# Performance work log

Hardware: AMD Instinct MI355X
Metric: run time of the kernel (lower is better)

Reference implementation:

```python
import jax, jax.numpy as jnp
import numpy as np

NUM_HEADS = 16
EMBED_DIM = 1024
HEAD_DIM = EMBED_DIM // NUM_HEADS


def setup_inputs() -> dict:
    key = jax.random.key(0)
    kq, kk, kv, kw, kb = jax.random.split(key, 5)
    B, S, D = 2, 2048, EMBED_DIM
    bound = 1.0 / np.sqrt(D)
    return {
        "query": jax.random.normal(kq, (B, S, D), dtype=jnp.float32),
        "key": jax.random.normal(kk, (B, S, D), dtype=jnp.float32),
        "value": jax.random.normal(kv, (B, S, D), dtype=jnp.float32),
        "W_out": jax.random.uniform(kw, (D, D), minval=-bound, maxval=bound, dtype=jnp.float32),
        "b_out": jax.random.uniform(kb, (D,), minval=-bound, maxval=bound, dtype=jnp.float32),
        "prelu_a": jnp.array(0.25, dtype=jnp.float32),
    }


def reference(query, key, value, W_out, b_out, prelu_a):
    B, S, D = query.shape
    # Note: the original forward never applies q/k/v linear layers, only reshape.
    q = query.reshape(B, S, NUM_HEADS, HEAD_DIM)  # b s h d
    k = key.reshape(B, S, NUM_HEADS, HEAD_DIM)
    v = value.reshape(B, S, NUM_HEADS, HEAD_DIM)
    scale = 1.0 / np.sqrt(HEAD_DIM).astype(np.float32)
    scores = jnp.einsum("bqhd,bkhd->bhqk", q, k) * scale  # [B,H,S,S]
    attn = jax.nn.softmax(scores, axis=-1)
    out = jnp.einsum("bhqk,bkhd->bqhd", attn, v).reshape(B, S, D)
    out = out @ W_out.T + b_out  # torch Linear: x @ W.T + b
    # dropout is identity in eval mode; PReLU with single scalar param
    out = jnp.where(out >= 0, out, prelu_a * out)
    return out
```

## Files before the change

### kernel.cpp

```cpp
#include <hip/hip_runtime.h>
#include <hip/hip_bf16.h>

typedef __attribute__((ext_vector_type(8))) short bf16x8;
typedef __attribute__((ext_vector_type(4))) float f32x4;

#define S_LEN 2048
#define EMB   1024
#define NH    16
#define HD    64

__device__ inline int swz(int row, int chunk) {
  return row * 64 + ((chunk ^ (row & 7)) << 3);
}

__device__ inline int swz128(int row, int chunk) {
  return row * 128 + ((chunk ^ (row & 15)) << 3);
}

__device__ inline int kperm(int s) {
  return (s & 0x23) | ((s & 0x04) << 2) | ((s & 0x18) >> 1);
}

__device__ inline uint4 cvt8(const float* __restrict__ src, float scale) {
  float4 f0 = ((const float4*)src)[0];
  float4 f1 = ((const float4*)src)[1];
  __hip_bfloat16 t[8];
  t[0] = __float2bfloat16(f0.x * scale);
  t[1] = __float2bfloat16(f0.y * scale);
  t[2] = __float2bfloat16(f0.z * scale);
  t[3] = __float2bfloat16(f0.w * scale);
  t[4] = __float2bfloat16(f1.x * scale);
  t[5] = __float2bfloat16(f1.y * scale);
  t[6] = __float2bfloat16(f1.z * scale);
  t[7] = __float2bfloat16(f1.w * scale);
  return *(uint4*)t;
}

__device__ inline uint4 cvt8r(float4 f0, float4 f1) {
  __hip_bfloat16 t[8];
  t[0] = __float2bfloat16(f0.x);
  t[1] = __float2bfloat16(f0.y);
  t[2] = __float2bfloat16(f0.z);
  t[3] = __float2bfloat16(f0.w);
  t[4] = __float2bfloat16(f1.x);
  t[5] = __float2bfloat16(f1.y);
  t[6] = __float2bfloat16(f1.z);
  t[7] = __float2bfloat16(f1.w);
  return *(uint4*)t;
}

__device__ inline void ld8f(const float* __restrict__ p, float4& a, float4& b) {
  a = ((const float4*)p)[0];
  b = ((const float4*)p)[1];
}

__global__ __launch_bounds__(256)
void prep(const float* __restrict__ V, __hip_bfloat16* __restrict__ Vt) {
  __shared__ float vt[64 * 65];
  const int tid = threadIdx.x;
  const int st = blockIdx.x, h = blockIdx.y, b = blockIdx.z;
  const size_t srcbase = ((size_t)(b * S_LEN + st * 64)) * EMB + h * HD;
  const size_t vtb = ((size_t)(b * NH + h) * HD) * S_LEN + st * 64;

  for (int c = tid; c < 512; c += 256) {
    const int r = c >> 3, c8 = (c & 7) * 8;
    const float* vsrc = V + srcbase + (size_t)r * EMB + c8;
    float4 a = ((const float4*)vsrc)[0];
    float4 d4 = ((const float4*)vsrc)[1];
    float tv[8] = {a.x, a.y, a.z, a.w, d4.x, d4.y, d4.z, d4.w};
    #pragma unroll
    for (int j = 0; j < 8; ++j) vt[r * 65 + c8 + j] = tv[j];
  }
  __syncthreads();
  for (int c = tid; c < 512; c += 256) {
    const int d = c >> 3, s8 = (c & 7) * 8;
    __hip_bfloat16 t[8];
    #pragma unroll
    for (int j = 0; j < 8; ++j)
      t[j] = __float2bfloat16(vt[(s8 + j) * 65 + d]);
    *(uint4*)(Vt + vtb + (size_t)d * S_LEN + s8) = *(uint4*)t;
  }
}

__global__ __launch_bounds__(512, 4)
void attn_fwd(const float* __restrict__ Q,
              const float* __restrict__ K,
              const __hip_bfloat16* __restrict__ Vt,
              __hip_bfloat16* __restrict__ O)
{
  __shared__ __align__(16) __hip_bfloat16 qs[128 * 64];
  __shared__ __align__(16) __hip_bfloat16 ks[2][128 * 64];
  __shared__ __align__(16) __hip_bfloat16 vs[2][64 * 128];

  const int qt   = blockIdx.x;
  const int h    = blockIdx.y;
  const int b    = blockIdx.z;
  const int tid  = threadIdx.x;
  const int wave = tid >> 6;
  const int lane = tid & 63;
  const int ln   = lane & 15;
  const int qd   = lane >> 4;

  const size_t baseQ = ((size_t)(b * S_LEN + qt * 128)) * EMB + h * HD;
  const size_t baseK = ((size_t)(b * S_LEN)) * EMB + h * HD;
  const size_t vtb   = ((size_t)(b * NH + h) * HD) * S_LEN;

  const int r0 = tid >> 3, cc = tid & 7;
  const int kpos0 = swz(kperm(r0), cc);
  const int kpos1 = kpos0 + 64 * 64;
  const int vr0 = tid >> 4, vch = tid & 15;
  const int vpos0 = swz128(vr0, vch);
  const int vpos1 = vpos0 + 32 * 128;

  float4 ka0, kb0, ka1, kb1;
  ld8f(K + baseK + (size_t)(r0)      * EMB + cc * 8, ka0, kb0);
  ld8f(K + baseK + (size_t)(64 + r0) * EMB + cc * 8, ka1, kb1);
  uint4 vreg0 = *(const uint4*)(Vt + vtb + (size_t)vr0        * S_LEN + vch * 8);
  uint4 vreg1 = *(const uint4*)(Vt + vtb + (size_t)(vr0 + 32) * S_LEN + vch * 8);

  const float qscale = 0.125f * 1.44269504088896f;
  #pragma unroll
  for (int i = 0; i < 2; ++i) {
    const int c = tid + 512 * i, row = c >> 3, ch = c & 7;
    *(uint4*)&qs[swz(row, ch)] = cvt8(Q + baseQ + (size_t)row * EMB + ch * 8, qscale);
  }
  *(uint4*)&ks[0][kpos0] = cvt8r(ka0, kb0);
  *(uint4*)&ks[0][kpos1] = cvt8r(ka1, kb1);
  *(uint4*)&vs[0][vpos0] = vreg0;
  *(uint4*)&vs[0][vpos1] = vreg1;
  ld8f(K + baseK + (size_t)(128 + r0) * EMB + cc * 8, ka0, kb0);
  ld8f(K + baseK + (size_t)(192 + r0) * EMB + cc * 8, ka1, kb1);
  vreg0 = *(const uint4*)(Vt + vtb + (size_t)vr0        * S_LEN + 128 + vch * 8);
  vreg1 = *(const uint4*)(Vt + vtb + (size_t)(vr0 + 32) * S_LEN + 128 + vch * 8);
  __syncthreads();

  bf16x8 aq[2];
  #pragma unroll
  for (int kh = 0; kh < 2; ++kh)
    aq[kh] = *(const bf16x8*)&qs[swz(wave * 16 + ln, kh * 4 + qd)];

  bf16x8 ones;
  #pragma unroll
  for (int j = 0; j < 8; ++j) ones[j] = (short)0x3F80;

  f32x4 oacc[4] = {};
  f32x4 lacc = {};

  for (int kt = 0; kt < S_LEN / 128; ++kt) {
    const int cur = kt & 1;
    if (kt + 1 < S_LEN / 128) {
      *(uint4*)&ks[1 - cur][kpos0] = cvt8r(ka0, kb0);
      *(uint4*)&ks[1 - cur][kpos1] = cvt8r(ka1, kb1);
      *(uint4*)&vs[1 - cur][vpos0] = vreg0;
      *(uint4*)&vs[1 - cur][vpos1] = vreg1;
      if (kt + 2 < S_LEN / 128) {
        const int kb2 = (kt + 2) * 128;
        ld8f(K + baseK + (size_t)(kb2 + r0)      * EMB + cc * 8, ka0, kb0);
        ld8f(K + baseK + (size_t)(kb2 + 64 + r0) * EMB + cc * 8, ka1, kb1);
        vreg0 = *(const uint4*)(Vt + vtb + (size_t)vr0        * S_LEN + kb2 + vch * 8);
        vreg1 = *(const uint4*)(Vt + vtb + (size_t)(vr0 + 32) * S_LEN + kb2 + vch * 8);
      }
    }

    f32x4 sfA[4], sfB[4];
    __builtin_amdgcn_s_setprio(1);
    #pragma unroll
    for (int k16 = 0; k16 < 4; ++k16) {
      const int krow = k16 * 16 + ln;
      bf16x8 ak0 = *(const bf16x8*)&ks[cur][swz(krow, qd)];
      bf16x8 ak1 = *(const bf16x8*)&ks[cur][swz(krow, 4 + qd)];
      f32x4 acc = {};
      acc = __builtin_amdgcn_mfma_f32_16x16x32_bf16(ak0, aq[0], acc, 0, 0, 0);
      sfA[k16] = __builtin_amdgcn_mfma_f32_16x16x32_bf16(ak1, aq[1], acc, 0, 0, 0);
    }
    #pragma unroll
    for (int k16 = 0; k16 < 4; ++k16) {
      const int krow = (4 + k16) * 16 + ln;
      bf16x8 ak0 = *(const bf16x8*)&ks[cur][swz(krow, qd)];
      bf16x8 ak1 = *(const bf16x8*)&ks[cur][swz(krow, 4 + qd)];
      f32x4 acc = {};
      acc = __builtin_amdgcn_mfma_f32_16x16x32_bf16(ak0, aq[0], acc, 0, 0, 0);
      sfB[k16] = __builtin_amdgcn_mfma_f32_16x16x32_bf16(ak1, aq[1], acc, 0, 0, 0);
    }
    __builtin_amdgcn_s_setprio(0);

    bf16x8 apA[2];
    #pragma unroll
    for (int t2 = 0; t2 < 2; ++t2)
      #pragma unroll
      for (int j = 0; j < 8; ++j) {
        const float p = __builtin_amdgcn_exp2f(sfA[t2 * 2 + (j >> 2)][j & 3]);
        __hip_bfloat16 hb = __float2bfloat16(p);
        apA[t2][j] = *(short*)&hb;
      }

    __builtin_amdgcn_s_setprio(1);
    #pragma unroll
    for (int t = 0; t < 2; ++t) {
      lacc = __builtin_amdgcn_mfma_f32_16x16x32_bf16(apA[t], ones, lacc, 0, 0, 0);
      #pragma unroll
      for (int dn = 0; dn < 4; ++dn) {
        bf16x8 bv = *(const bf16x8*)&vs[cur][swz128(dn * 16 + ln, t * 4 + qd)];
        oacc[dn] = __builtin_amdgcn_mfma_f32_16x16x32_bf16(apA[t], bv, oacc[dn], 0, 0, 0);
      }
    }
    __builtin_amdgcn_s_setprio(0);

    bf16x8 apB[2];
    #pragma unroll
    for (int t2 = 0; t2 < 2; ++t2)
      #pragma unroll
      for (int j = 0; j < 8; ++j) {
        const float p = __builtin_amdgcn_exp2f(sfB[t2 * 2 + (j >> 2)][j & 3]);
        __hip_bfloat16 hb = __float2bfloat16(p);
        apB[t2][j] = *(short*)&hb;
      }

    __builtin_amdgcn_s_setprio(1);
    #pragma unroll
    for (int t = 0; t < 2; ++t) {
      lacc = __builtin_amdgcn_mfma_f32_16x16x32_bf16(apB[t], ones, lacc, 0, 0, 0);
      #pragma unroll
      for (int dn = 0; dn < 4; ++dn) {
        bf16x8 bv = *(const bf16x8*)&vs[cur][swz128(dn * 16 + ln, (2 + t) * 4 + qd)];
        oacc[dn] = __builtin_amdgcn_mfma_f32_16x16x32_bf16(apB[t], bv, oacc[dn], 0, 0, 0);
      }
    }
    __builtin_amdgcn_s_setprio(0);

    __syncthreads();
  }

  #pragma unroll
  for (int r = 0; r < 4; ++r) {
    const float inv = 1.f / lacc[r];
    const int row = wave * 16 + qd * 4 + r;
    #pragma unroll
    for (int dn = 0; dn < 4; ++dn)
      O[baseQ + (size_t)row * EMB + dn * 16 + ln] =
          __float2bfloat16(oacc[dn][r] * inv);
  }
}

__global__ __launch_bounds__(256, 2)
void proj_prelu(const __hip_bfloat16* __restrict__ X,
                const float* __restrict__ W,
                const float* __restrict__ Bv,
                const float* __restrict__ Pa,
                float* __restrict__ Out)
{
  __shared__ __align__(16) __hip_bfloat16 xs[2][128 * 64];
  __shared__ __align__(16) __hip_bfloat16 wsm[2][64 * 64];

  const int m0   = blockIdx.x * 128;
  const int n0   = blockIdx.y * 64;
  const int tid  = threadIdx.x;
  const int wave = tid >> 6;
  const int wm   = wave >> 1;
  const int wn   = wave & 1;
  const int lane = tid & 63;
  const int ln   = lane & 15;
  const int qd   = lane >> 4;

  const int r0 = tid >> 3, cc = tid & 7;

  f32x4 acc[8] = {};

  uint4 xg0, xg1, xg2, xg3;
  float4 wa0, wb0, wa1, wb1;
  #define LOADK(ko)                                                           \
    xg0 = *(const uint4*)(X  + (size_t)(m0 + r0     ) * EMB + (ko) + cc * 8); \
    xg1 = *(const uint4*)(X  + (size_t)(m0 + r0 + 32) * EMB + (ko) + cc * 8); \
    xg2 = *(const uint4*)(X  + (size_t)(m0 + r0 + 64) * EMB + (ko) + cc * 8); \
    xg3 = *(const uint4*)(X  + (size_t)(m0 + r0 + 96) * EMB + (ko) + cc * 8); \
    ld8f(W + (size_t)(n0 + r0     ) * EMB + (ko) + cc * 8, wa0, wb0);         \
    ld8f(W + (size_t)(n0 + r0 + 32) * EMB + (ko) + cc * 8, wa1, wb1)
  #define STORELDS(buf)                                                       \
    *(uint4*)&xs [buf][swz(r0,      cc)] = xg0;                               \
    *(uint4*)&xs [buf][swz(r0 + 32, cc)] = xg1;                               \
    *(uint4*)&xs [buf][swz(r0 + 64, cc)] = xg2;                               \
    *(uint4*)&xs [buf][swz(r0 + 96, cc)] = xg3;                               \
    *(uint4*)&wsm[buf][swz(r0,      cc)] = cvt8r(wa0, wb0);                   \
    *(uint4*)&wsm[buf][swz(r0 + 32, cc)] = cvt8r(wa1, wb1)

  LOADK(0);
  STORELDS(0);
  LOADK(64);
  __syncthreads();

  for (int kt = 0; kt < EMB / 64; ++kt) {
    const int cur = kt & 1;
    if (kt + 1 < EMB / 64) {
      STORELDS(1 - cur);
      if (kt + 2 < EMB / 64) {
        LOADK((kt + 2) * 64);
      }
    }

    #pragma unroll
    for (int ks2 = 0; ks2 < 2; ++ks2) {
      bf16x8 ax0 = *(const bf16x8*)&xs[cur][swz(wm * 64 +  0 + ln, ks2 * 4 + qd)];
      bf16x8 ax1 = *(const bf16x8*)&xs[cur][swz(wm * 64 + 16 + ln, ks2 * 4 + qd)];
      bf16x8 ax2 = *(const bf16x8*)&xs[cur][swz(wm * 64 + 32 + ln, ks2 * 4 + qd)];
      bf16x8 ax3 = *(const bf16x8*)&xs[cur][swz(wm * 64 + 48 + ln, ks2 * 4 + qd)];
      bf16x8 bw0 = *(const bf16x8*)&wsm[cur][swz(wn * 32 +  0 + ln, ks2 * 4 + qd)];
      bf16x8 bw1 = *(const bf16x8*)&wsm[cur][swz(wn * 32 + 16 + ln, ks2 * 4 + qd)];
      acc[0] = __builtin_amdgcn_mfma_f32_16x16x32_bf16(ax0, bw0, acc[0], 0, 0, 0);
      acc[1] = __builtin_amdgcn_mfma_f32_16x16x32_bf16(ax0, bw1, acc[1], 0, 0, 0);
      acc[2] = __builtin_amdgcn_mfma_f32_16x16x32_bf16(ax1, bw0, acc[2], 0, 0, 0);
      acc[3] = __builtin_amdgcn_mfma_f32_16x16x32_bf16(ax1, bw1, acc[3], 0, 0, 0);
      acc[4] = __builtin_amdgcn_mfma_f32_16x16x32_bf16(ax2, bw0, acc[4], 0, 0, 0);
      acc[5] = __builtin_amdgcn_mfma_f32_16x16x32_bf16(ax2, bw1, acc[5], 0, 0, 0);
      acc[6] = __builtin_amdgcn_mfma_f32_16x16x32_bf16(ax3, bw0, acc[6], 0, 0, 0);
      acc[7] = __builtin_amdgcn_mfma_f32_16x16x32_bf16(ax3, bw1, acc[7], 0, 0, 0);
    }
    __syncthreads();
  }

  const float a = Pa[0];
  #pragma unroll
  for (int mf = 0; mf < 4; ++mf) {
    #pragma unroll
    for (int nf = 0; nf < 2; ++nf) {
      const float bn = Bv[n0 + wn * 32 + nf * 16 + ln];
      #pragma unroll
      for (int r = 0; r < 4; ++r) {
        float y = acc[mf * 2 + nf][r] + bn;
        y = (y >= 0.f) ? y : a * y;
        Out[(size_t)(m0 + wm * 64 + mf * 16 + qd * 4 + r) * EMB +
            n0 + wn * 32 + nf * 16 + ln] = y;
      }
    }
  }
  #undef LOADK
  #undef STORELDS
}

extern "C" void kernel_launch(void* const* d_in, const int* in_sizes, int n_in,
                              void* d_out, int out_size, void* d_ws, size_t ws_size,
                              hipStream_t stream) {
  const float* Q  = (const float*)d_in[0];
  const float* K  = (const float*)d_in[1];
  const float* V  = (const float*)d_in[2];
  const float* W  = (const float*)d_in[3];
  const float* Bb = (const float*)d_in[4];
  const float* Pa = (const float*)d_in[5];
  float* Out = (float*)d_out;

  char* ws = (char*)d_ws;
  __hip_bfloat16* Xws = (__hip_bfloat16*)(ws);
  __hip_bfloat16* Vt  = (__hip_bfloat16*)(ws + (16u << 20));

  prep      <<<dim3(S_LEN / 64, NH, 2), 256, 0, stream>>>(V, Vt);
  attn_fwd  <<<dim3(S_LEN / 128, NH, 2), 512, 0, stream>>>(Q, K, Vt, Xws);
  proj_prelu<<<dim3(2 * S_LEN / 128, EMB / 64), 256, 0, stream>>>(Xws, W, Bb, Pa, Out);
}
```

Baseline: 156.2 us.

## Pre-convert K to bf16 in prep and software-pipeline PV across iterations

The prep kernel now also converts K to a head-major bf16 buffer, so the attention kernel loads half the bytes per K tile and skips the per-iteration fp32-to-bf16 conversion. The attention loop is also software-pipelined: the second half's P·V MFMAs are deferred to the next iteration, with their V fragments held in registers. This lets them interleave with the next QK^T and exp work, and a drain step after the loop finishes the last tile. The cost is extra registers (8 bf16x8 V fragments plus the P fragments), which may raise register pressure under the 4-blocks-per-SM launch bound. It also adds an extra global write and read of K in bf16.

```diff
diff --git a/kernel.cpp b/kernel.cpp
--- a/kernel.cpp
+++ b/kernel.cpp
@@ -55,15 +55,18 @@
 }
 
 __global__ __launch_bounds__(256)
-void prep(const float* __restrict__ V, __hip_bfloat16* __restrict__ Vt) {
+void prep(const float* __restrict__ K, const float* __restrict__ V,
+          __hip_bfloat16* __restrict__ Kb, __hip_bfloat16* __restrict__ Vt) {
   __shared__ float vt[64 * 65];
   const int tid = threadIdx.x;
   const int st = blockIdx.x, h = blockIdx.y, b = blockIdx.z;
   const size_t srcbase = ((size_t)(b * S_LEN + st * 64)) * EMB + h * HD;
+  const size_t kvb = ((size_t)(b * NH + h) * S_LEN + st * 64) * HD;
   const size_t vtb = ((size_t)(b * NH + h) * HD) * S_LEN + st * 64;
 
   for (int c = tid; c < 512; c += 256) {
     const int r = c >> 3, c8 = (c & 7) * 8;
+    *(uint4*)(Kb + kvb + r * HD + c8) = cvt8(K + srcbase + (size_t)r * EMB + c8, 1.0f);
     const float* vsrc = V + srcbase + (size_t)r * EMB + c8;
     float4 a = ((const float4*)vsrc)[0];
     float4 d4 = ((const float4*)vsrc)[1];
@@ -84,7 +87,7 @@
 
 __global__ __launch_bounds__(512, 4)
 void attn_fwd(const float* __restrict__ Q,
-              const float* __restrict__ K,
+              const __hip_bfloat16* __restrict__ Kb,
               const __hip_bfloat16* __restrict__ Vt,
               __hip_bfloat16* __restrict__ O)
 {
@@ -102,7 +105,7 @@
   const int qd   = lane >> 4;
 
   const size_t baseQ = ((size_t)(b * S_LEN + qt * 128)) * EMB + h * HD;
-  const size_t baseK = ((size_t)(b * S_LEN)) * EMB + h * HD;
+  const size_t kvb   = ((size_t)(b * NH + h) * S_LEN) * HD;
   const size_t vtb   = ((size_t)(b * NH + h) * HD) * S_LEN;
 
   const int r0 = tid >> 3, cc = tid & 7;
@@ -112,9 +115,8 @@
   const int vpos0 = swz128(vr0, vch);
   const int vpos1 = vpos0 + 32 * 128;
 
-  float4 ka0, kb0, ka1, kb1;
-  ld8f(K + baseK + (size_t)(r0)      * EMB + cc * 8, ka0, kb0);
-  ld8f(K + baseK + (size_t)(64 + r0) * EMB + cc * 8, ka1, kb1);
+  uint4 kreg0 = *(const uint4*)(Kb + kvb + (size_t)(r0)       * HD + cc * 8);
+  uint4 kreg1 = *(const uint4*)(Kb + kvb + (size_t)(64 + r0)  * HD + cc * 8);
   uint4 vreg0 = *(const uint4*)(Vt + vtb + (size_t)vr0        * S_LEN + vch * 8);
   uint4 vreg1 = *(const uint4*)(Vt + vtb + (size_t)(vr0 + 32) * S_LEN + vch * 8);
 
@@ -124,12 +126,12 @@
     const int c = tid + 512 * i, row = c >> 3, ch = c & 7;
     *(uint4*)&qs[swz(row, ch)] = cvt8(Q + baseQ + (size_t)row * EMB + ch * 8, qscale);
   }
-  *(uint4*)&ks[0][kpos0] = cvt8r(ka0, kb0);
-  *(uint4*)&ks[0][kpos1] = cvt8r(ka1, kb1);
+  *(uint4*)&ks[0][kpos0] = kreg0;
+  *(uint4*)&ks[0][kpos1] = kreg1;
   *(uint4*)&vs[0][vpos0] = vreg0;
   *(uint4*)&vs[0][vpos1] = vreg1;
-  ld8f(K + baseK + (size_t)(128 + r0) * EMB + cc * 8, ka0, kb0);
-  ld8f(K + baseK + (size_t)(192 + r0) * EMB + cc * 8, ka1, kb1);
+  kreg0 = *(const uint4*)(Kb + kvb + (size_t)(128 + r0)      * HD + cc * 8);
+  kreg1 = *(const uint4*)(Kb + kvb + (size_t)(192 + r0)      * HD + cc * 8);
   vreg0 = *(const uint4*)(Vt + vtb + (size_t)vr0        * S_LEN + 128 + vch * 8);
   vreg1 = *(const uint4*)(Vt + vtb + (size_t)(vr0 + 32) * S_LEN + 128 + vch * 8);
   __syncthreads();
@@ -145,24 +147,26 @@
 
   f32x4 oacc[4] = {};
   f32x4 lacc = {};
+  bf16x8 apD[2] = {};
+  bf16x8 bvD[8] = {};
 
   for (int kt = 0; kt < S_LEN / 128; ++kt) {
     const int cur = kt & 1;
     if (kt + 1 < S_LEN / 128) {
-      *(uint4*)&ks[1 - cur][kpos0] = cvt8r(ka0, kb0);
-      *(uint4*)&ks[1 - cur][kpos1] = cvt8r(ka1, kb1);
+      *(uint4*)&ks[1 - cur][kpos0] = kreg0;
+      *(uint4*)&ks[1 - cur][kpos1] = kreg1;
       *(uint4*)&vs[1 - cur][vpos0] = vreg0;
       *(uint4*)&vs[1 - cur][vpos1] = vreg1;
       if (kt + 2 < S_LEN / 128) {
         const int kb2 = (kt + 2) * 128;
-        ld8f(K + baseK + (size_t)(kb2 + r0)      * EMB + cc * 8, ka0, kb0);
-        ld8f(K + baseK + (size_t)(kb2 + 64 + r0) * EMB + cc * 8, ka1, kb1);
+        kreg0 = *(const uint4*)(Kb + kvb + (size_t)(kb2 + r0)       * HD + cc * 8);
+        kreg1 = *(const uint4*)(Kb + kvb + (size_t)(kb2 + 64 + r0)  * HD + cc * 8);
         vreg0 = *(const uint4*)(Vt + vtb + (size_t)vr0        * S_LEN + kb2 + vch * 8);
         vreg1 = *(const uint4*)(Vt + vtb + (size_t)(vr0 + 32) * S_LEN + kb2 + vch * 8);
       }
     }
 
-    f32x4 sfA[4], sfB[4];
+    f32x4 sfA[4];
     __builtin_amdgcn_s_setprio(1);
     #pragma unroll
     for (int k16 = 0; k16 < 4; ++k16) {
@@ -173,6 +177,27 @@
       acc = __builtin_amdgcn_mfma_f32_16x16x32_bf16(ak0, aq[0], acc, 0, 0, 0);
       sfA[k16] = __builtin_amdgcn_mfma_f32_16x16x32_bf16(ak1, aq[1], acc, 0, 0, 0);
     }
+    __builtin_amdgcn_s_setprio(0);
+
+    bf16x8 apA[2];
+    #pragma unroll
+    for (int t2 = 0; t2 < 2; ++t2)
+      #pragma unroll
+      for (int j = 0; j < 8; ++j) {
+        const float p = __builtin_amdgcn_exp2f(sfA[t2 * 2 + (j >> 2)][j & 3]);
+        __hip_bfloat16 hb = __float2bfloat16(p);
+        apA[t2][j] = *(short*)&hb;
+      }
+
+    f32x4 sfB[4];
+    __builtin_amdgcn_s_setprio(1);
+    #pragma unroll
+    for (int t = 0; t < 2; ++t) {
+      lacc = __builtin_amdgcn_mfma_f32_16x16x32_bf16(apD[t], ones, lacc, 0, 0, 0);
+      #pragma unroll
+      for (int dn = 0; dn < 4; ++dn)
+        oacc[dn] = __builtin_amdgcn_mfma_f32_16x16x32_bf16(apD[t], bvD[t * 4 + dn], oacc[dn], 0, 0, 0);
+    }
     #pragma unroll
     for (int k16 = 0; k16 < 4; ++k16) {
       const int krow = (4 + k16) * 16 + ln;
@@ -184,28 +209,6 @@
     }
     __builtin_amdgcn_s_setprio(0);
 
-    bf16x8 apA[2];
-    #pragma unroll
-    for (int t2 = 0; t2 < 2; ++t2)
-      #pragma unroll
-      for (int j = 0; j < 8; ++j) {
-        const float p = __builtin_amdgcn_exp2f(sfA[t2 * 2 + (j >> 2)][j & 3]);
-        __hip_bfloat16 hb = __float2bfloat16(p);
-        apA[t2][j] = *(short*)&hb;
-      }
-
-    __builtin_amdgcn_s_setprio(1);
-    #pragma unroll
-    for (int t = 0; t < 2; ++t) {
-      lacc = __builtin_amdgcn_mfma_f32_16x16x32_bf16(apA[t], ones, lacc, 0, 0, 0);
-      #pragma unroll
-      for (int dn = 0; dn < 4; ++dn) {
-        bf16x8 bv = *(const bf16x8*)&vs[cur][swz128(dn * 16 + ln, t * 4 + qd)];
-        oacc[dn] = __builtin_amdgcn_mfma_f32_16x16x32_bf16(apA[t], bv, oacc[dn], 0, 0, 0);
-      }
-    }
-    __builtin_amdgcn_s_setprio(0);
-
     bf16x8 apB[2];
     #pragma unroll
     for (int t2 = 0; t2 < 2; ++t2)
@@ -219,18 +222,33 @@
     __builtin_amdgcn_s_setprio(1);
     #pragma unroll
     for (int t = 0; t < 2; ++t) {
-      lacc = __builtin_amdgcn_mfma_f32_16x16x32_bf16(apB[t], ones, lacc, 0, 0, 0);
+      lacc = __builtin_amdgcn_mfma_f32_16x16x32_bf16(apA[t], ones, lacc, 0, 0, 0);
       #pragma unroll
       for (int dn = 0; dn < 4; ++dn) {
-        bf16x8 bv = *(const bf16x8*)&vs[cur][swz128(dn * 16 + ln, (2 + t) * 4 + qd)];
-        oacc[dn] = __builtin_amdgcn_mfma_f32_16x16x32_bf16(apB[t], bv, oacc[dn], 0, 0, 0);
+        bf16x8 bv = *(const bf16x8*)&vs[cur][swz128(dn * 16 + ln, t * 4 + qd)];
+        oacc[dn] = __builtin_amdgcn_mfma_f32_16x16x32_bf16(apA[t], bv, oacc[dn], 0, 0, 0);
       }
     }
     __builtin_amdgcn_s_setprio(0);
 
+    #pragma unroll
+    for (int t = 0; t < 2; ++t)
+      #pragma unroll
+      for (int dn = 0; dn < 4; ++dn)
+        bvD[t * 4 + dn] = *(const bf16x8*)&vs[cur][swz128(dn * 16 + ln, (2 + t) * 4 + qd)];
+    apD[0] = apB[0];
+    apD[1] = apB[1];
+
     __syncthreads();
   }
 
+  #pragma unroll
+  for (int t = 0; t < 2; ++t) {
+    lacc = __builtin_amdgcn_mfma_f32_16x16x32_bf16(apD[t], ones, lacc, 0, 0, 0);
+    #pragma unroll
+    for (int dn = 0; dn < 4; ++dn)
+      oacc[dn] = __builtin_amdgcn_mfma_f32_16x16x32_bf16(apD[t], bvD[t * 4 + dn], oacc[dn], 0, 0, 0);
+  }
   #pragma unroll
   for (int r = 0; r < 4; ++r) {
     const float inv = 1.f / lacc[r];
@@ -349,9 +367,10 @@
 
   char* ws = (char*)d_ws;
   __hip_bfloat16* Xws = (__hip_bfloat16*)(ws);
+  __hip_bfloat16* Kb  = (__hip_bfloat16*)(ws + (8u  << 20));
   __hip_bfloat16* Vt  = (__hip_bfloat16*)(ws + (16u << 20));
 
-  prep      <<<dim3(S_LEN / 64, NH, 2), 256, 0, stream>>>(V, Vt);
-  attn_fwd  <<<dim3(S_LEN / 128, NH, 2), 512, 0, stream>>>(Q, K, Vt, Xws);
+  prep      <<<dim3(S_LEN / 64, NH, 2), 256, 0, stream>>>(K, V, Kb, Vt);
+  attn_fwd  <<<dim3(S_LEN / 128, NH, 2), 512, 0, stream>>>(Q, Kb, Vt, Xws);
   proj_prelu<<<dim3(2 * S_LEN / 128, EMB / 64), 256, 0, stream>>>(Xws, W, Bb, Pa, Out);
 }
```

Measured after the change: 155.9 us. About the same (-0.2%).
